# Kernel tuning notes

Measured on AMD Instinct MI355X. Metric: run time of the kernel, lower is better.

Reference implementation:

```python
import jax, jax.numpy as jnp
import numpy as np

N_NODES = 50000
N_EDGES = 800000
NUM_RELATIONS = 8   # 2 * n_speakers**2 with n_speakers = 2
NUM_BASES = 30
G_DIM, H1_DIM, H2_DIM = 128, 128, 128


def setup_inputs() -> dict:
    key = jax.random.key(0)
    ks = jax.random.split(key, 10)
    inp = {
        "node_features": jax.random.normal(ks[0], (N_NODES, G_DIM), jnp.float32),
        "edge_index": jax.random.randint(ks[1], (2, N_EDGES), 0, N_NODES, dtype=jnp.int64),
        "edge_type": jax.random.randint(ks[2], (N_EDGES,), 0, NUM_RELATIONS, dtype=jnp.int64),
        "edge_norm": jax.random.uniform(ks[3], (N_EDGES,), jnp.float32),
        # RGCNConv params (basis decomposition)
        "basis": jax.random.normal(ks[4], (NUM_BASES, G_DIM, H1_DIM), jnp.float32) * 0.05,
        "comp": jax.random.normal(ks[5], (NUM_RELATIONS, NUM_BASES), jnp.float32) * 0.1,
        "root": jax.random.normal(ks[6], (G_DIM, H1_DIM), jnp.float32) * 0.05,
        "bias1": jnp.zeros((H1_DIM,), jnp.float32),
        # GraphConv params: lin_rel (with bias) applied to aggregated neighbors, lin_root (no bias)
        "w_rel": jax.random.normal(ks[7], (H1_DIM, H2_DIM), jnp.float32) * 0.05,
        "b_rel": jnp.zeros((H2_DIM,), jnp.float32),
        "w_root": jax.random.normal(ks[8], (H1_DIM, H2_DIM), jnp.float32) * 0.05,
    }
    return inp


def reference(node_features, edge_index, edge_type, edge_norm,
              basis, comp, root, bias1, w_rel, b_rel, w_root):
    src, dst = edge_index[0], edge_index[1]  # source_to_target flow (PyG default)

    # ---- Layer 1: RGCNConv with basis decomposition ----
    # W[r] = sum_b comp[r,b] * basis[b]  -> [R, g, h1]
    W = jnp.einsum('rb,bio->rio', comp, basis)
    # Project every node under every relation once (N*R*h1), then gather per edge.
    # Mathematically identical to per-edge x_j @ W[edge_type] but avoids an [E, g, h1] tensor.
    x_proj = jnp.einsum('ni,rio->nro', node_features, W)  # [N, R, h1]
    msg = x_proj[src, edge_type] * edge_norm[:, None]     # [E, h1]
    agg = jax.ops.segment_sum(msg, dst, num_segments=N_NODES)  # scatter-add to targets
    h = agg + node_features @ root + bias1                # [N, h1]

    # ---- Layer 2: GraphConv (aggr='add', no edge_weight) ----
    agg2 = jax.ops.segment_sum(h[src], dst, num_segments=N_NODES)  # [N, h1]
    out = agg2 @ w_rel + b_rel + h @ w_root               # [N, h2]
    return out
```

## Files before the change

### kernel.cpp

```cpp
#include <hip/hip_runtime.h>
#include <hip/hip_bf16.h>
#include <stdint.h>

#define N_NODES 50000
#define N_EDGES 800000
#define NREL    8
#define NBASES  30
#define DIM     128
#define NKEYS   (N_NODES * NREL)
#define KFULL   1152
#define SCAN_NB ((NKEYS + 255) / 256)

typedef __attribute__((ext_vector_type(8))) short short8;
typedef __attribute__((ext_vector_type(4))) float floatx4;
typedef __hip_bfloat16  bf16;
typedef __hip_bfloat162 bf16x2;

__device__ inline ushort f2bu(float f) { bf16 b = __float2bfloat16(f); return *(ushort*)&b; }
__device__ inline float  bu2f(ushort u) { union { unsigned i; float f; } c; c.i = ((unsigned)u) << 16; return c.f; }

__global__ void prep_weights(const float* __restrict__ basis, const float* __restrict__ comp,
                             const float* __restrict__ root, const float* __restrict__ w_rel,
                             const float* __restrict__ w_root,
                             bf16* __restrict__ WfullT, bf16* __restrict__ wrelT, bf16* __restrict__ wrootT) {
    int idx = blockIdx.x * blockDim.x + threadIdx.x;
    const int n_full = DIM * KFULL;
    const int n_sq   = DIM * DIM;
    if (idx < n_full) {
        int k = idx % KFULL, o = idx / KFULL;
        float v;
        if (k < 1024) {
            int r = k >> 7, i = k & 127;
            v = 0.f;
            for (int b = 0; b < NBASES; ++b)
                v += comp[r * NBASES + b] * basis[(b * DIM + i) * DIM + o];
        } else {
            v = root[(k - 1024) * DIM + o];
        }
        WfullT[o * KFULL + k] = __float2bfloat16(v);
    } else if (idx < n_full + n_sq) {
        int t = idx - n_full; int k = t & 127, o = t >> 7;
        wrelT[o * DIM + k] = __float2bfloat16(w_rel[k * DIM + o]);
    } else if (idx < n_full + 2 * n_sq) {
        int t = idx - n_full - n_sq; int k = t & 127, o = t >> 7;
        wrootT[o * DIM + k] = __float2bfloat16(w_root[k * DIM + o]);
    }
}

__global__ void conv_x(const float4* __restrict__ x4, ushort4* __restrict__ xb4, int n4) {
    int i = blockIdx.x * blockDim.x + threadIdx.x;
    if (i < n4) {
        float4 f = x4[i];
        ushort4 o;
        o.x = f2bu(f.x); o.y = f2bu(f.y); o.z = f2bu(f.z); o.w = f2bu(f.w);
        xb4[i] = o;
    }
}

__global__ void hist_kernel(const int* __restrict__ ei, const int* __restrict__ et,
                            int* __restrict__ deg) {
    int e = blockIdx.x * blockDim.x + threadIdx.x;
    if (e < N_EDGES) atomicAdd(&deg[ei[N_EDGES + e] * NREL + et[e]], 1);
}

__global__ void scan_blocks(const int* __restrict__ deg, int* __restrict__ segoff,
                            int* __restrict__ bsum, int n) {
    __shared__ int buf[256];
    int tid = threadIdx.x;
    int i = blockIdx.x * 256 + tid;
    int v = (i < n) ? deg[i] : 0;
    buf[tid] = v;
    __syncthreads();
#pragma unroll
    for (int o = 1; o < 256; o <<= 1) {
        int t = (tid >= o) ? buf[tid - o] : 0;
        __syncthreads();
        buf[tid] += t;
        __syncthreads();
    }
    if (i < n) segoff[i + 1] = buf[tid];
    if (tid == 255) bsum[blockIdx.x] = buf[255];
}

__global__ void scan_sums(int* __restrict__ bsum, int nb) {
    int lane = threadIdx.x;
    int base = 0;
    for (int start = 0; start < nb; start += 64) {
        int i = start + lane;
        int v = (i < nb) ? bsum[i] : 0;
        int incl = v;
#pragma unroll
        for (int o = 1; o < 64; o <<= 1) {
            int t = __shfl_up(incl, o, 64);
            if (lane >= o) incl += t;
        }
        if (i < nb) bsum[i] = base + incl - v;
        base += __shfl(incl, 63, 64);
    }
}

__global__ void scan_add(int* __restrict__ segoff, const int* __restrict__ bsum, int n) {
    int i = blockIdx.x * 256 + threadIdx.x;
    if (i < n) segoff[i + 1] += bsum[blockIdx.x];
    if (i == 0) segoff[0] = 0;
}

__global__ void scatter_kernel(const int* __restrict__ ei, const int* __restrict__ et,
                               const float* __restrict__ en, const int* __restrict__ segoff,
                               int* __restrict__ cur, uint2* __restrict__ rec) {
    int e = blockIdx.x * blockDim.x + threadIdx.x;
    if (e < N_EDGES) {
        int typ = et[e];
        int key = ei[N_EDGES + e] * NREL + typ;
        int p = segoff[key] + atomicAdd(&cur[key], 1);
        rec[p] = make_uint2((unsigned)ei[e] | ((unsigned)typ << 16), __float_as_uint(en[e]));
    }
}

__global__ void agg1_kernel(const uint2* __restrict__ rec, const int* __restrict__ segoff,
                            const ushort* __restrict__ xb, ushort* __restrict__ agg) {
    int quad = threadIdx.x >> 4;
    int node = blockIdx.x * 16 + quad;
    if (node >= N_NODES) return;
    int lane = threadIdx.x & 15;
    int base = node * NREL;
    int s = segoff[base], e = segoff[base + NREL];
    float acc[8] = {0.f, 0.f, 0.f, 0.f, 0.f, 0.f, 0.f, 0.f};
    int cur_t = 0;
    for (int chunk = s; chunk < e; chunk += 4) {
        int m = e - chunk; if (m > 4) m = 4;
        uint2 rr[4]; short8 vv[4];
#pragma unroll
        for (int j = 0; j < 4; ++j) if (j < m) rr[j] = rec[chunk + j];
#pragma unroll
        for (int j = 0; j < 4; ++j) if (j < m)
            vv[j] = *(const short8*)(xb + (size_t)(rr[j].x & 0xFFFFu) * 128 + lane * 8);
#pragma unroll
        for (int j = 0; j < 4; ++j) if (j < m) {
            int t = (int)(rr[j].x >> 16);
            if (t != cur_t) {
                short8 o;
#pragma unroll
                for (int f = 0; f < 8; ++f) o[f] = (short)f2bu(acc[f]);
                *(short8*)(agg + (size_t)(base + cur_t) * 128 + lane * 8) = o;
                short8 z = {0, 0, 0, 0, 0, 0, 0, 0};
                for (int tt = cur_t + 1; tt < t; ++tt)
                    *(short8*)(agg + (size_t)(base + tt) * 128 + lane * 8) = z;
#pragma unroll
                for (int f = 0; f < 8; ++f) acc[f] = 0.f;
                cur_t = t;
            }
            float norm = __uint_as_float(rr[j].y);
#pragma unroll
            for (int f = 0; f < 8; ++f) acc[f] += norm * bu2f((ushort)vv[j][f]);
        }
    }
    {
        short8 o;
#pragma unroll
        for (int f = 0; f < 8; ++f) o[f] = (short)f2bu(acc[f]);
        *(short8*)(agg + (size_t)(base + cur_t) * 128 + lane * 8) = o;
        short8 z = {0, 0, 0, 0, 0, 0, 0, 0};
        for (int tt = cur_t + 1; tt < NREL; ++tt)
            *(short8*)(agg + (size_t)(base + tt) * 128 + lane * 8) = z;
    }
}

__global__ __launch_bounds__(256) void gemm_h(const bf16* __restrict__ agg, const bf16* __restrict__ xb,
                                              const bf16* __restrict__ WfullT, const float* __restrict__ bias1,
                                              bf16* __restrict__ h, int M) {
    __shared__ ushort As[64][72];
    __shared__ ushort Bs[128][72];
    const ushort* Au_agg = (const ushort*)agg;
    const ushort* Au_x   = (const ushort*)xb;
    const ushort* Bu     = (const ushort*)WfullT;
    int tm = blockIdx.x * 64;
    int wave = threadIdx.x >> 6, lane = threadIdx.x & 63;
    int q = lane >> 4, mr = lane & 15;
    floatx4 zero = {0.f, 0.f, 0.f, 0.f};
    floatx4 acc[8] = {zero, zero, zero, zero, zero, zero, zero, zero};

    for (int kt = 0; kt < 18; ++kt) {
        if (kt) __syncthreads();
#pragma unroll
        for (int u = 0; u < 2; ++u) {
            int cc = threadIdx.x + u * 256;
            int row = cc >> 3, seg = cc & 7;
            int gr = tm + row;
            short8 av = {0, 0, 0, 0, 0, 0, 0, 0};
            if (gr < M) {
                if (kt < 16) av = *(const short8*)(Au_agg + (size_t)gr * 1024 + kt * 64 + seg * 8);
                else         av = *(const short8*)(Au_x   + (size_t)gr * 128 + (kt - 16) * 64 + seg * 8);
            }
            *(short8*)(&As[row][seg * 8]) = av;
        }
#pragma unroll
        for (int u = 0; u < 4; ++u) {
            int cc = threadIdx.x + u * 256;
            int row = cc >> 3, seg = cc & 7;
            short8 bv = *(const short8*)(Bu + (size_t)row * KFULL + kt * 64 + seg * 8);
            *(short8*)(&Bs[row][seg * 8]) = bv;
        }
        __syncthreads();
#pragma unroll
        for (int kh = 0; kh < 2; ++kh) {
            short8 a = *(const short8*)(&As[wave * 16 + mr][q * 8 + kh * 32]);
#pragma unroll
            for (int nt = 0; nt < 8; ++nt) {
                short8 b = *(const short8*)(&Bs[nt * 16 + mr][q * 8 + kh * 32]);
                acc[nt] = __builtin_amdgcn_mfma_f32_16x16x32_bf16(a, b, acc[nt], 0, 0, 0);
            }
        }
    }
#pragma unroll
    for (int nt = 0; nt < 8; ++nt)
#pragma unroll
        for (int r4 = 0; r4 < 4; ++r4) {
            int row = tm + wave * 16 + q * 4 + r4;
            int col = nt * 16 + mr;
            if (row < M) h[(size_t)row * 128 + col] = __float2bfloat16(acc[nt][r4] + bias1[col]);
        }
}

__global__ void seg2_kernel(const uint2* __restrict__ rec, const int* __restrict__ segoff,
                            const ushort* __restrict__ h, ushort* __restrict__ out2) {
    int quad = threadIdx.x >> 4;
    int node = blockIdx.x * 16 + quad;
    if (node >= N_NODES) return;
    int lane = threadIdx.x & 15;
    int s = segoff[node * NREL], e = segoff[node * NREL + NREL];
    float acc[8] = {0.f, 0.f, 0.f, 0.f, 0.f, 0.f, 0.f, 0.f};
    for (int chunk = s; chunk < e; chunk += 4) {
        int m = e - chunk; if (m > 4) m = 4;
        uint2 rr[4]; short8 vv[4];
#pragma unroll
        for (int j = 0; j < 4; ++j) if (j < m) rr[j] = rec[chunk + j];
#pragma unroll
        for (int j = 0; j < 4; ++j) if (j < m)
            vv[j] = *(const short8*)(h + (size_t)(rr[j].x & 0xFFFFu) * 128 + lane * 8);
#pragma unroll
        for (int j = 0; j < 4; ++j) if (j < m)
#pragma unroll
            for (int f = 0; f < 8; ++f) acc[f] += bu2f((ushort)vv[j][f]);
    }
    short8 o;
#pragma unroll
    for (int f = 0; f < 8; ++f) o[f] = (short)f2bu(acc[f]);
    *(short8*)(out2 + (size_t)node * 128 + lane * 8) = o;
}

__global__ __launch_bounds__(256) void gemm2_kernel(const bf16* __restrict__ A1, const bf16* __restrict__ B1T,
                                                    const bf16* __restrict__ A2, const bf16* __restrict__ B2T,
                                                    const float* __restrict__ brel, float* __restrict__ out, int M) {
    __shared__ ushort As[64][136];
    __shared__ ushort Bs[64][136];
    int tm = blockIdx.x * 64, tn = blockIdx.y * 64;
    int wave = threadIdx.x >> 6, lane = threadIdx.x & 63;
    int q = lane >> 4, mr = lane & 15;
    floatx4 zero = {0.f, 0.f, 0.f, 0.f};
    floatx4 acc[4] = {zero, zero, zero, zero};

    for (int phase = 0; phase < 2; ++phase) {
        const ushort* Au = (const ushort*)(phase ? A2 : A1);
        const ushort* Bu = (const ushort*)(phase ? B2T : B1T);
        if (phase) __syncthreads();
        for (int c = threadIdx.x; c < 64 * 16; c += 256) {
            int row = c >> 4, seg = c & 15;
            int gr = tm + row;
            short8 av = {0, 0, 0, 0, 0, 0, 0, 0};
            if (gr < M) av = *(const short8*)(Au + (size_t)gr * 128 + seg * 8);
            *(short8*)(&As[row][seg * 8]) = av;
            short8 bv = *(const short8*)(Bu + (size_t)(tn + row) * 128 + seg * 8);
            *(short8*)(&Bs[row][seg * 8]) = bv;
        }
        __syncthreads();
#pragma unroll
        for (int kt = 0; kt < 4; ++kt) {
            short8 a = *(const short8*)(&As[wave * 16 + mr][q * 8 + kt * 32]);
#pragma unroll
            for (int nt = 0; nt < 4; ++nt) {
                short8 b = *(const short8*)(&Bs[nt * 16 + mr][q * 8 + kt * 32]);
                acc[nt] = __builtin_amdgcn_mfma_f32_16x16x32_bf16(a, b, acc[nt], 0, 0, 0);
            }
        }
    }
#pragma unroll
    for (int nt = 0; nt < 4; ++nt)
#pragma unroll
        for (int r4 = 0; r4 < 4; ++r4) {
            int row = tm + wave * 16 + q * 4 + r4;
            int col = tn + nt * 16 + mr;
            if (row < M) out[(size_t)row * 128 + col] = acc[nt][r4] + brel[col];
        }
}

extern "C" void kernel_launch(void* const* d_in, const int* in_sizes, int n_in,
                              void* d_out, int out_size, void* d_ws, size_t ws_size,
                              hipStream_t stream) {
    const float* x      = (const float*)d_in[0];
    const int*   ei     = (const int*)d_in[1];
    const int*   et     = (const int*)d_in[2];
    const float* en     = (const float*)d_in[3];
    const float* basis  = (const float*)d_in[4];
    const float* comp   = (const float*)d_in[5];
    const float* root   = (const float*)d_in[6];
    const float* bias1  = (const float*)d_in[7];
    const float* w_rel  = (const float*)d_in[8];
    const float* b_rel  = (const float*)d_in[9];
    const float* w_root = (const float*)d_in[10];
    float* out = (float*)d_out;

    char* ws = (char*)d_ws;
    size_t off = 0;
    auto alloc = [&](size_t bytes) { size_t o = off; off += (bytes + 255) & ~(size_t)255; return o; };

    size_t o_deg    = alloc((size_t)NKEYS * 4);
    size_t o_cur    = alloc((size_t)NKEYS * 4);
    size_t o_segoff = alloc((size_t)(NKEYS + 1) * 4);
    size_t o_bsum   = alloc((size_t)SCAN_NB * 4);
    size_t o_rec    = alloc((size_t)N_EDGES * 8);
    size_t o_wfull  = alloc((size_t)DIM * KFULL * 2);
    size_t o_wrel   = alloc((size_t)DIM * DIM * 2);
    size_t o_wroot  = alloc((size_t)DIM * DIM * 2);
    size_t o_xb     = alloc((size_t)N_NODES * DIM * 2);
    size_t o_agg    = alloc((size_t)N_NODES * NREL * DIM * 2);
    size_t o_hb     = alloc((size_t)N_NODES * DIM * 2);
    size_t o_agg2   = alloc((size_t)N_NODES * DIM * 2);

    int*   deg    = (int*)(ws + o_deg);
    int*   cur    = (int*)(ws + o_cur);
    int*   segoff = (int*)(ws + o_segoff);
    int*   bsum   = (int*)(ws + o_bsum);
    uint2* rec    = (uint2*)(ws + o_rec);
    bf16*  wfull  = (bf16*)(ws + o_wfull);
    bf16*  wrelT  = (bf16*)(ws + o_wrel);
    bf16*  wrootT = (bf16*)(ws + o_wroot);
    bf16*  xb     = (bf16*)(ws + o_xb);
    bf16*  agg    = (bf16*)(ws + o_agg);
    bf16*  hb     = (bf16*)(ws + o_hb);
    bf16*  agg2   = (bf16*)(ws + o_agg2);

    hipMemsetAsync(ws + o_deg, 0, o_segoff - o_deg, stream);

    {
        int total = DIM * KFULL + 2 * DIM * DIM;
        prep_weights<<<(total + 255) / 256, 256, 0, stream>>>(basis, comp, root, w_rel, w_root,
                                                              wfull, wrelT, wrootT);
    }
    {
        int n4 = N_NODES * DIM / 4;
        conv_x<<<(n4 + 255) / 256, 256, 0, stream>>>((const float4*)x, (ushort4*)xb, n4);
    }
    hist_kernel<<<(N_EDGES + 255) / 256, 256, 0, stream>>>(ei, et, deg);
    scan_blocks<<<SCAN_NB, 256, 0, stream>>>(deg, segoff, bsum, NKEYS);
    scan_sums<<<1, 64, 0, stream>>>(bsum, SCAN_NB);
    scan_add<<<SCAN_NB, 256, 0, stream>>>(segoff, bsum, NKEYS);
    scatter_kernel<<<(N_EDGES + 255) / 256, 256, 0, stream>>>(ei, et, en, segoff, cur, rec);

    agg1_kernel<<<(N_NODES + 15) / 16, 256, 0, stream>>>(rec, segoff, (const ushort*)xb, (ushort*)agg);
    gemm_h<<<(N_NODES + 63) / 64, 256, 0, stream>>>(agg, xb, wfull, bias1, hb, N_NODES);
    seg2_kernel<<<(N_NODES + 15) / 16, 256, 0, stream>>>(rec, segoff, (const ushort*)hb, (ushort*)agg2);
    {
        dim3 grid((N_NODES + 63) / 64, DIM / 64);
        gemm2_kernel<<<grid, 256, 0, stream>>>(agg2, wrelT, hb, wrootT, b_rel, out, N_NODES);
    }
}
```

Baseline: 364.5 us.

## Fuse per-relation edge aggregation into layer-1 GEMM, dropping agg buffer

Replaces the separate agg1 kernel, which wrote an [N,8,128] bf16 aggregate to global memory, and the gemm_h kernel that read it back. The new kernel gathers the neighbour rows for each relation directly into shared memory and feeds them to MFMA with a K-tile of 128, one tile per relation plus a final root tile. This removes about 100MB of global write and read traffic. In exchange the gather now runs inside the GEMM block with only 64 nodes per block and syncs between the gather and MFMA phases, which may hurt latency hiding and occupancy because the shared-memory tiles are larger.

```diff
diff --git a/kernel.cpp b/kernel.cpp
--- a/kernel.cpp
+++ b/kernel.cpp
@@ -117,97 +117,75 @@
     }
 }
 
-__global__ void agg1_kernel(const uint2* __restrict__ rec, const int* __restrict__ segoff,
-                            const ushort* __restrict__ xb, ushort* __restrict__ agg) {
-    int quad = threadIdx.x >> 4;
-    int node = blockIdx.x * 16 + quad;
-    if (node >= N_NODES) return;
-    int lane = threadIdx.x & 15;
-    int base = node * NREL;
-    int s = segoff[base], e = segoff[base + NREL];
-    float acc[8] = {0.f, 0.f, 0.f, 0.f, 0.f, 0.f, 0.f, 0.f};
-    int cur_t = 0;
-    for (int chunk = s; chunk < e; chunk += 4) {
-        int m = e - chunk; if (m > 4) m = 4;
-        uint2 rr[4]; short8 vv[4];
-#pragma unroll
-        for (int j = 0; j < 4; ++j) if (j < m) rr[j] = rec[chunk + j];
-#pragma unroll
-        for (int j = 0; j < 4; ++j) if (j < m)
-            vv[j] = *(const short8*)(xb + (size_t)(rr[j].x & 0xFFFFu) * 128 + lane * 8);
-#pragma unroll
-        for (int j = 0; j < 4; ++j) if (j < m) {
-            int t = (int)(rr[j].x >> 16);
-            if (t != cur_t) {
-                short8 o;
-#pragma unroll
-                for (int f = 0; f < 8; ++f) o[f] = (short)f2bu(acc[f]);
-                *(short8*)(agg + (size_t)(base + cur_t) * 128 + lane * 8) = o;
-                short8 z = {0, 0, 0, 0, 0, 0, 0, 0};
-                for (int tt = cur_t + 1; tt < t; ++tt)
-                    *(short8*)(agg + (size_t)(base + tt) * 128 + lane * 8) = z;
-#pragma unroll
-                for (int f = 0; f < 8; ++f) acc[f] = 0.f;
-                cur_t = t;
-            }
-            float norm = __uint_as_float(rr[j].y);
-#pragma unroll
-            for (int f = 0; f < 8; ++f) acc[f] += norm * bu2f((ushort)vv[j][f]);
-        }
-    }
-    {
-        short8 o;
-#pragma unroll
-        for (int f = 0; f < 8; ++f) o[f] = (short)f2bu(acc[f]);
-        *(short8*)(agg + (size_t)(base + cur_t) * 128 + lane * 8) = o;
-        short8 z = {0, 0, 0, 0, 0, 0, 0, 0};
-        for (int tt = cur_t + 1; tt < NREL; ++tt)
-            *(short8*)(agg + (size_t)(base + tt) * 128 + lane * 8) = z;
-    }
-}
-
-__global__ __launch_bounds__(256) void gemm_h(const bf16* __restrict__ agg, const bf16* __restrict__ xb,
-                                              const bf16* __restrict__ WfullT, const float* __restrict__ bias1,
-                                              bf16* __restrict__ h, int M) {
-    __shared__ ushort As[64][72];
-    __shared__ ushort Bs[128][72];
-    const ushort* Au_agg = (const ushort*)agg;
-    const ushort* Au_x   = (const ushort*)xb;
-    const ushort* Bu     = (const ushort*)WfullT;
+__global__ __launch_bounds__(256) void fused_h(const uint2* __restrict__ rec, const int* __restrict__ segoff,
+                                               const ushort* __restrict__ xb, const ushort* __restrict__ WfullT,
+                                               const float* __restrict__ bias1, ushort* __restrict__ h, int M) {
+    __shared__ ushort As[64][136];
+    __shared__ ushort Bs[128][136];
+    int tid = threadIdx.x;
     int tm = blockIdx.x * 64;
-    int wave = threadIdx.x >> 6, lane = threadIdx.x & 63;
+    int wave = tid >> 6, lane = tid & 63;
     int q = lane >> 4, mr = lane & 15;
+    int quad = tid >> 4;
+    int ql = tid & 15;
     floatx4 zero = {0.f, 0.f, 0.f, 0.f};
     floatx4 acc[8] = {zero, zero, zero, zero, zero, zero, zero, zero};
 
-    for (int kt = 0; kt < 18; ++kt) {
-        if (kt) __syncthreads();
-#pragma unroll
-        for (int u = 0; u < 2; ++u) {
-            int cc = threadIdx.x + u * 256;
-            int row = cc >> 3, seg = cc & 7;
-            int gr = tm + row;
-            short8 av = {0, 0, 0, 0, 0, 0, 0, 0};
-            if (gr < M) {
-                if (kt < 16) av = *(const short8*)(Au_agg + (size_t)gr * 1024 + kt * 64 + seg * 8);
-                else         av = *(const short8*)(Au_x   + (size_t)gr * 128 + (kt - 16) * 64 + seg * 8);
+    for (int r = 0; r < 9; ++r) {
+        if (r) __syncthreads();
+        if (r < 8) {
+            for (int i = 0; i < 4; ++i) {
+                int n_local = quad * 4 + i;
+                int node = tm + n_local;
+                float acf[8] = {0.f, 0.f, 0.f, 0.f, 0.f, 0.f, 0.f, 0.f};
+                if (node < M) {
+                    int s = segoff[node * NREL + r], e = segoff[node * NREL + r + 1];
+                    for (int chunk = s; chunk < e; chunk += 4) {
+                        int m = e - chunk; if (m > 4) m = 4;
+                        uint2 rr[4]; short8 vv[4];
+#pragma unroll
+                        for (int j = 0; j < 4; ++j) if (j < m) rr[j] = rec[chunk + j];
+#pragma unroll
+                        for (int j = 0; j < 4; ++j) if (j < m)
+                            vv[j] = *(const short8*)(xb + (size_t)(rr[j].x & 0xFFFFu) * 128 + ql * 8);
+#pragma unroll
+                        for (int j = 0; j < 4; ++j) if (j < m) {
+                            float norm = __uint_as_float(rr[j].y);
+#pragma unroll
+                            for (int f = 0; f < 8; ++f) acf[f] += norm * bu2f((ushort)vv[j][f]);
+                        }
+                    }
+                }
+                short8 o;
+#pragma unroll
+                for (int f = 0; f < 8; ++f) o[f] = (short)f2bu(acf[f]);
+                *(short8*)(&As[n_local][ql * 8]) = o;
             }
-            *(short8*)(&As[row][seg * 8]) = av;
-        }
-#pragma unroll
-        for (int u = 0; u < 4; ++u) {
-            int cc = threadIdx.x + u * 256;
-            int row = cc >> 3, seg = cc & 7;
-            short8 bv = *(const short8*)(Bu + (size_t)row * KFULL + kt * 64 + seg * 8);
+        } else {
+#pragma unroll
+            for (int u = 0; u < 4; ++u) {
+                int cc = tid + u * 256;
+                int row = cc >> 4, seg = cc & 15;
+                int gr = tm + row;
+                short8 av = {0, 0, 0, 0, 0, 0, 0, 0};
+                if (gr < M) av = *(const short8*)(xb + (size_t)gr * 128 + seg * 8);
+                *(short8*)(&As[row][seg * 8]) = av;
+            }
+        }
+#pragma unroll
+        for (int u = 0; u < 8; ++u) {
+            int cc = tid + u * 256;
+            int row = cc >> 4, seg = cc & 15;
+            short8 bv = *(const short8*)(WfullT + (size_t)row * KFULL + r * 128 + seg * 8);
             *(short8*)(&Bs[row][seg * 8]) = bv;
         }
         __syncthreads();
 #pragma unroll
-        for (int kh = 0; kh < 2; ++kh) {
-            short8 a = *(const short8*)(&As[wave * 16 + mr][q * 8 + kh * 32]);
+        for (int ks = 0; ks < 4; ++ks) {
+            short8 a = *(const short8*)(&As[wave * 16 + mr][q * 8 + ks * 32]);
 #pragma unroll
             for (int nt = 0; nt < 8; ++nt) {
-                short8 b = *(const short8*)(&Bs[nt * 16 + mr][q * 8 + kh * 32]);
+                short8 b = *(const short8*)(&Bs[nt * 16 + mr][q * 8 + ks * 32]);
                 acc[nt] = __builtin_amdgcn_mfma_f32_16x16x32_bf16(a, b, acc[nt], 0, 0, 0);
             }
         }
@@ -218,7 +196,7 @@
         for (int r4 = 0; r4 < 4; ++r4) {
             int row = tm + wave * 16 + q * 4 + r4;
             int col = nt * 16 + mr;
-            if (row < M) h[(size_t)row * 128 + col] = __float2bfloat16(acc[nt][r4] + bias1[col]);
+            if (row < M) h[(size_t)row * 128 + col] = f2bu(acc[nt][r4] + bias1[col]);
         }
 }
 
@@ -323,7 +301,6 @@
     size_t o_wrel   = alloc((size_t)DIM * DIM * 2);
     size_t o_wroot  = alloc((size_t)DIM * DIM * 2);
     size_t o_xb     = alloc((size_t)N_NODES * DIM * 2);
-    size_t o_agg    = alloc((size_t)N_NODES * NREL * DIM * 2);
     size_t o_hb     = alloc((size_t)N_NODES * DIM * 2);
     size_t o_agg2   = alloc((size_t)N_NODES * DIM * 2);
 
@@ -336,7 +313,6 @@
     bf16*  wrelT  = (bf16*)(ws + o_wrel);
     bf16*  wrootT = (bf16*)(ws + o_wroot);
     bf16*  xb     = (bf16*)(ws + o_xb);
-    bf16*  agg    = (bf16*)(ws + o_agg);
     bf16*  hb     = (bf16*)(ws + o_hb);
     bf16*  agg2   = (bf16*)(ws + o_agg2);
 
@@ -357,8 +333,8 @@
     scan_add<<<SCAN_NB, 256, 0, stream>>>(segoff, bsum, NKEYS);
     scatter_kernel<<<(N_EDGES + 255) / 256, 256, 0, stream>>>(ei, et, en, segoff, cur, rec);
 
-    agg1_kernel<<<(N_NODES + 15) / 16, 256, 0, stream>>>(rec, segoff, (const ushort*)xb, (ushort*)agg);
-    gemm_h<<<(N_NODES + 63) / 64, 256, 0, stream>>>(agg, xb, wfull, bias1, hb, N_NODES);
+    fused_h<<<(N_NODES + 63) / 64, 256, 0, stream>>>(rec, segoff, (const ushort*)xb,
+                                                     (const ushort*)wfull, bias1, (ushort*)hb, N_NODES);
     seg2_kernel<<<(N_NODES + 15) / 16, 256, 0, stream>>>(rec, segoff, (const ushort*)hb, (ushort*)agg2);
     {
         dim3 grid((N_NODES + 63) / 64, DIM / 64);
```

New measurement: 461.8 us. 26.7% more time.
